# Performance work log

Measured on AMD Instinct MI355X. Metric: run time of the kernel, lower is better.

## Reference

```python
import jax, jax.numpy as jnp
import numpy as np

NODE = 112
L1, L2, L3 = 256, 128, 64
BATCH = 2048


def setup_inputs() -> dict:
    key = jax.random.key(0)
    ks = jax.random.split(key, 19)
    def n(k, shape, s=0.05):
        return jax.random.normal(k, shape, jnp.float32) * s
    return {
        "x": jax.random.uniform(ks[0], (BATCH, NODE, NODE), jnp.float32),
        # GAT1: proj Linear(112->L1); attention Linear(2*L1->1) split into (wa1, wb1, ba1)
        "Wp1": n(ks[1], (L1, NODE)), "bp1": n(ks[2], (L1,)),
        "wa1": n(ks[3], (L1,)), "wb1": n(ks[4], (L1,)), "ba1": n(ks[5], ()),
        # Pool1: proj Linear(L1->1)
        "Wpool1": n(ks[6], (L1,)), "bpool1": n(ks[7], ()),
        # GAT2
        "Wp2": n(ks[8], (L2, L1)), "bp2": n(ks[9], (L2,)),
        "wa2": n(ks[10], (L2,)), "wb2": n(ks[11], (L2,)), "ba2": n(ks[12], ()),
        # Pool2
        "Wpool2": n(ks[13], (L2,)), "bpool2": n(ks[14], ()),
        # FC head
        "Wfc1": n(ks[15], (L3, L2)), "bfc1": n(ks[16], (L3,)),
        "Wfc2": n(ks[17], (1, L3)), "bfc2": n(ks[18], (1,)),
    }


def _gat(a, h, Wp, bp, wa, wb, ba):
    # h: [B,N,Din] -> [B,N,O]
    h = jnp.einsum('bnd,od->bno', h, Wp) + bp
    # attention(concat(h_i, h_j)) == h_i.wa + h_j.wb + ba (linear over concat splits)
    s = jnp.einsum('bno,o->bn', h, wa)  # first-half contribution
    t = jnp.einsum('bno,o->bn', h, wb)  # second-half contribution
    e = jax.nn.relu(s[:, :, None] + t[:, None, :] + ba)  # [B,N,N]
    att = jnp.exp(e) * a
    att = att / jnp.sum(att, axis=-1, keepdims=True)
    return jnp.einsum('bij,bjo->bio', att, h) + h


def _pool(adj, hidden, w, b, k):
    scores = jax.nn.sigmoid(jnp.einsum('bnd,d->bn', hidden, w) + b)  # [B,N]
    vals, idx = jax.lax.top_k(scores, k)  # sorted descending, like torch.topk
    hidden = jnp.take_along_axis(hidden, idx[:, :, None], axis=1) * vals[:, :, None]
    adj = jnp.take_along_axis(adj, idx[:, :, None], axis=1)
    adj = jnp.take_along_axis(adj, idx[:, None, :], axis=2)
    adj = adj / jnp.sum(adj, axis=-1, keepdims=True)
    return adj, hidden


def reference(x, Wp1, bp1, wa1, wb1, ba1, Wpool1, bpool1,
              Wp2, bp2, wa2, wb2, ba2, Wpool2, bpool2,
              Wfc1, bfc1, Wfc2, bfc2):
    b = x.shape[0]
    h = jnp.broadcast_to(jnp.eye(NODE, dtype=x.dtype), (b, NODE, NODE))
    h = jax.nn.relu(_gat(x, h, Wp1, bp1, wa1, wb1, ba1))
    k1 = max(2, int(0.5 * NODE))          # 56
    a, h = _pool(x, h, Wpool1, bpool1, k1)
    h = jax.nn.relu(_gat(a, h, Wp2, bp2, wa2, wb2, ba2))
    k2 = max(2, int(0.5 * k1))            # 28
    a, h = _pool(a, h, Wpool2, bpool2, k2)
    h = jnp.mean(h, axis=1)               # [B,L2]
    h = jax.nn.relu(h @ Wfc1.T + bfc1)
    return h @ Wfc2.T + bfc2              # [B,1]
```

## Files before the change

kernel.cpp:

```cpp
#include <hip/hip_runtime.h>

#define NODE 112
#define KP1 56
#define KP2 28
#define D1 256
#define D2 128
#define NBATCH 2048
#define NCH 4
#define WR 7
#define GR 7
#define CR 28

typedef const float* __restrict__ fp;

__global__ void k0a(fp Wp1, fp bp1, fp wa1, fp wb1,
                    float* __restrict__ s1, float* __restrict__ t1)
{
    int tid = threadIdx.x;
    int i = tid >> 1, half = tid & 1;
    float sa = 0.f, sb = 0.f;
    if (i < NODE) {
        for (int o = half*128; o < half*128 + 128; o++) {
            float h = Wp1[o*NODE + i] + bp1[o];
            sa += h * wa1[o];
            sb += h * wb1[o];
        }
    }
    sa += __shfl_xor(sa, 1, 64);
    sb += __shfl_xor(sb, 1, 64);
    if (i < NODE && half == 0) { s1[i] = sa; t1[i] = sb; }
}

__global__ void k0b(fp Wp1, fp bp1, fp ba1, fp Wp2,
                    const float* __restrict__ s1, const float* __restrict__ t1,
                    float* __restrict__ hp, float* __restrict__ E1, float* __restrict__ W2T)
{
    int g = blockIdx.x*blockDim.x + threadIdx.x;
    int stride = gridDim.x*blockDim.x;
    for (int e = g; e < NODE*D1; e += stride) {
        int j = e >> 8, o = e & 255;
        hp[e] = Wp1[o*NODE + j] + bp1[o];
    }
    float ba = ba1[0];
    for (int e = g; e < NODE*NODE; e += stride) {
        int i = e / NODE, j = e - i*NODE;
        E1[e] = expf(fmaxf(s1[i] + t1[j] + ba, 0.f));
    }
    for (int e = g; e < D1*D2; e += stride) {
        int d = e >> 7, o = e & 127;
        W2T[e] = Wp2[o*D1 + d];
    }
}

__device__ __forceinline__ void topk_wave(volatile float* sc, int n, int k,
                                          int* idxo, float* valo, int tid)
{
    for (int it = 0; it < k; it++) {
        float v = (tid < n) ? sc[tid] : -1e30f;
        int bi = tid;
        int j2 = tid + 64;
        if (j2 < n) { float v2 = sc[j2]; if (v2 > v) { v = v2; bi = j2; } }
        #pragma unroll
        for (int off = 32; off; off >>= 1) {
            float ov = __shfl_xor(v, off, 64);
            int   oi = __shfl_xor(bi, off, 64);
            if (ov > v || (ov == v && oi < bi)) { v = ov; bi = oi; }
        }
        if (tid == 0) { idxo[it] = bi; valo[it] = v; sc[bi] = -1e30f; }
    }
}

__device__ __forceinline__ float sigm(float v) { return 1.f/(1.f + expf(-v)); }

__global__ __launch_bounds__(256, 2) void gnn_fast(
    fp x, fp Wpool1, fp bpool1, fp bp2, fp wa2, fp wb2, fp ba2,
    fp Wpool2, fp bpool2, fp Wfc1, fp bfc1, fp Wfc2, fp bfc2,
    fp hp, fp E1, fp W2T, float* __restrict__ out)
{
    __shared__ __align__(16) float ovl[KP1*D1];
    __shared__ __align__(16) float awc2[KP1*KP1];
    __shared__ float rinv[NODE];
    __shared__ float sc1[NODE];
    __shared__ int   idx1[KP1];
    __shared__ float vals1[KP1];
    __shared__ int   sel[NODE];
    __shared__ float s2v[KP1], t2v[KP1];
    __shared__ float rs2inv[KP1];
    __shared__ float sc2[KP1];
    __shared__ int   idx2[KP2];
    __shared__ float vals2[KP2];
    __shared__ float hmean[D2];

    float* awcF = ovl;
    float* hg   = ovl;

    const int tid = threadIdx.x;
    const int lane = tid & 63, wave = tid >> 6;
    const int b = blockIdx.x;
    const float* xb = x + (size_t)b*NODE*NODE;

    const float4 wp1v = *(const float4*)(Wpool1 + 4*lane);
    const float bpool1v = bpool1[0];

    {
        const int seg = tid & 3;
        #pragma unroll
        for (int pass = 0; pass < 2; pass++) {
            const int i = (tid >> 2) + pass*64;
            float ps = 0.f;
            if (i < NODE) {
                const float4* Er = (const float4*)(E1 + i*NODE + seg*28);
                const float4* xr = (const float4*)(xb + i*NODE + seg*28);
                float4* ar = (float4*)(awcF + i*NODE + seg*28);
                #pragma unroll
                for (int q = 0; q < 7; q++) {
                    float4 e = Er[q], xv = xr[q];
                    float4 v = make_float4(e.x*xv.x, e.y*xv.y, e.z*xv.z, e.w*xv.w);
                    ar[q] = v;
                    ps += (v.x + v.y) + (v.z + v.w);
                }
            }
            ps += __shfl_xor(ps, 1, 64);
            ps += __shfl_xor(ps, 2, 64);
            if (i < NODE && seg == 0) rinv[i] = 1.f/ps;
        }
    }
    __syncthreads();

    const int r0 = wave*WR;
    float h1r[NCH][WR][4];
    #pragma unroll
    for (int c = 0; c < NCH; c++) {
        float acc[WR][4];
        #pragma unroll
        for (int r = 0; r < WR; r++) { acc[r][0]=0.f; acc[r][1]=0.f; acc[r][2]=0.f; acc[r][3]=0.f; }
        #pragma unroll 2
        for (int jq = 0; jq < NODE/4; jq++) {
            const int j = jq*4;
            float4 hv0 = *(const float4*)(hp + (j+0)*D1 + 4*lane);
            float4 hv1 = *(const float4*)(hp + (j+1)*D1 + 4*lane);
            float4 hv2 = *(const float4*)(hp + (j+2)*D1 + 4*lane);
            float4 hv3 = *(const float4*)(hp + (j+3)*D1 + 4*lane);
            #pragma unroll
            for (int r = 0; r < WR; r++) {
                float4 a4 = *(const float4*)&awcF[(c*CR + r0 + r)*NODE + j];
                acc[r][0] += a4.x*hv0.x + a4.y*hv1.x + a4.z*hv2.x + a4.w*hv3.x;
                acc[r][1] += a4.x*hv0.y + a4.y*hv1.y + a4.z*hv2.y + a4.w*hv3.y;
                acc[r][2] += a4.x*hv0.z + a4.y*hv1.z + a4.z*hv2.z + a4.w*hv3.z;
                acc[r][3] += a4.x*hv0.w + a4.y*hv1.w + a4.z*hv2.w + a4.w*hv3.w;
            }
        }
        #pragma unroll
        for (int r = 0; r < WR; r++) {
            const int i = c*CR + r0 + r;
            const float ri = rinv[i];
            float4 hpi = *(const float4*)(hp + i*D1 + 4*lane);
            float v0 = fmaxf(acc[r][0]*ri + hpi.x, 0.f);
            float v1 = fmaxf(acc[r][1]*ri + hpi.y, 0.f);
            float v2 = fmaxf(acc[r][2]*ri + hpi.z, 0.f);
            float v3 = fmaxf(acc[r][3]*ri + hpi.w, 0.f);
            h1r[c][r][0]=v0; h1r[c][r][1]=v1; h1r[c][r][2]=v2; h1r[c][r][3]=v3;
            float p = v0*wp1v.x + v1*wp1v.y + v2*wp1v.z + v3*wp1v.w;
            #pragma unroll
            for (int off = 32; off; off >>= 1) p += __shfl_xor(p, off, 64);
            if (lane == 0) sc1[i] = sigm(p + bpool1v);
        }
    }
    __syncthreads();

    if (tid < 64) topk_wave(sc1, NODE, KP1, idx1, vals1, tid);
    else if (tid >= 128 && tid < 128 + NODE) sel[tid - 128] = -1;
    __syncthreads();
    if (tid < KP1) sel[idx1[tid]] = tid;
    __syncthreads();

    #pragma unroll
    for (int c = 0; c < NCH; c++) {
        #pragma unroll
        for (int r = 0; r < WR; r++) {
            const int i = c*CR + r0 + r;
            const int k = sel[i];
            if (k >= 0) {
                const float vs = vals1[k];
                *(float4*)&hg[k*D1 + 4*lane] =
                    make_float4(h1r[c][r][0]*vs, h1r[c][r][1]*vs,
                                h1r[c][r][2]*vs, h1r[c][r][3]*vs);
            }
        }
    }
    __syncthreads();

    {
        const int g = tid >> 5;
        const int cs = tid & 31;
        float acc2[GR][4];
        #pragma unroll
        for (int r = 0; r < GR; r++) { acc2[r][0]=0.f; acc2[r][1]=0.f; acc2[r][2]=0.f; acc2[r][3]=0.f; }
        #pragma unroll 2
        for (int dq = 0; dq < D1/4; dq++) {
            const int d = dq*4;
            float4 w0 = *(const float4*)(W2T + (d+0)*D2 + 4*cs);
            float4 w1 = *(const float4*)(W2T + (d+1)*D2 + 4*cs);
            float4 w2 = *(const float4*)(W2T + (d+2)*D2 + 4*cs);
            float4 w3 = *(const float4*)(W2T + (d+3)*D2 + 4*cs);
            #pragma unroll
            for (int r = 0; r < GR; r++) {
                float4 a4 = *(const float4*)&hg[(g*GR+r)*D1 + d];
                acc2[r][0] += a4.x*w0.x + a4.y*w1.x + a4.z*w2.x + a4.w*w3.x;
                acc2[r][1] += a4.x*w0.y + a4.y*w1.y + a4.z*w2.y + a4.w*w3.y;
                acc2[r][2] += a4.x*w0.z + a4.y*w1.z + a4.z*w2.z + a4.w*w3.z;
                acc2[r][3] += a4.x*w0.w + a4.y*w1.w + a4.z*w2.w + a4.w*w3.w;
            }
        }
        float4 b2 = *(const float4*)(bp2 + 4*cs);
        __syncthreads();
        #pragma unroll
        for (int r = 0; r < GR; r++) {
            *(float4*)&hg[(g*GR+r)*D1 + 4*cs] =
                make_float4(acc2[r][0]+b2.x, acc2[r][1]+b2.y, acc2[r][2]+b2.z, acc2[r][3]+b2.w);
        }
    }
    __syncthreads();

    if (tid < 4*KP1) {
        int row = tid >> 2, seg = tid & 3;
        float sa = 0.f, sb = 0.f;
        #pragma unroll
        for (int q = 0; q < 8; q++) {
            float4 hv = *(const float4*)&hg[row*D1 + seg*32 + q*4];
            float4 va = *(const float4*)(wa2 + seg*32 + q*4);
            float4 vb = *(const float4*)(wb2 + seg*32 + q*4);
            sa += hv.x*va.x + hv.y*va.y + hv.z*va.z + hv.w*va.w;
            sb += hv.x*vb.x + hv.y*vb.y + hv.z*vb.z + hv.w*vb.w;
        }
        sa += __shfl_xor(sa, 1, 64); sa += __shfl_xor(sa, 2, 64);
        sb += __shfl_xor(sb, 1, 64); sb += __shfl_xor(sb, 2, 64);
        if (seg == 0) { s2v[row] = sa; t2v[row] = sb; }
    }
    __syncthreads();

    if (tid < 4*KP1) {
        int rloc = tid >> 2, seg = tid & 3;
        float ps = 0.f;
        int gi = idx1[rloc];
        float srow = s2v[rloc];
        const float ba2v = ba2[0];
        const float* xrow = xb + gi*NODE;
        float* arow = awc2 + rloc*KP1 + seg*14;
        #pragma unroll
        for (int q = 0; q < 14; q++) {
            int j = seg*14 + q;
            float e = fmaxf(srow + t2v[j] + ba2v, 0.f);
            float v = expf(e) * xrow[idx1[j]];
            arow[q] = v;
            ps += v;
        }
        ps += __shfl_xor(ps, 1, 64); ps += __shfl_xor(ps, 2, 64);
        if (seg == 0) rs2inv[rloc] = 1.f/ps;
    }
    __syncthreads();

    {
        const int g = tid >> 5, cs = tid & 31;
        float acc3[GR][4];
        #pragma unroll
        for (int r = 0; r < GR; r++) { acc3[r][0]=0.f; acc3[r][1]=0.f; acc3[r][2]=0.f; acc3[r][3]=0.f; }
        #pragma unroll 2
        for (int lq = 0; lq < KP1/4; lq++) {
            const int l = lq*4;
            float4 p0 = *(const float4*)&hg[(l+0)*D1 + 4*cs];
            float4 p1 = *(const float4*)&hg[(l+1)*D1 + 4*cs];
            float4 p2 = *(const float4*)&hg[(l+2)*D1 + 4*cs];
            float4 p3 = *(const float4*)&hg[(l+3)*D1 + 4*cs];
            #pragma unroll
            for (int r = 0; r < GR; r++) {
                float4 a4 = *(const float4*)&awc2[(g*GR+r)*KP1 + l];
                acc3[r][0] += a4.x*p0.x + a4.y*p1.x + a4.z*p2.x + a4.w*p3.x;
                acc3[r][1] += a4.x*p0.y + a4.y*p1.y + a4.z*p2.y + a4.w*p3.y;
                acc3[r][2] += a4.x*p0.z + a4.y*p1.z + a4.z*p2.z + a4.w*p3.z;
                acc3[r][3] += a4.x*p0.w + a4.y*p1.w + a4.z*p2.w + a4.w*p3.w;
            }
        }
        const float4 wp2v = *(const float4*)(Wpool2 + 4*cs);
        const float bpool2v = bpool2[0];
        #pragma unroll
        for (int r = 0; r < GR; r++) {
            int row = g*GR + r;
            float ri = rs2inv[row];
            float4 hpj = *(const float4*)&hg[row*D1 + 4*cs];
            float v0 = fmaxf(acc3[r][0]*ri + hpj.x, 0.f);
            float v1 = fmaxf(acc3[r][1]*ri + hpj.y, 0.f);
            float v2 = fmaxf(acc3[r][2]*ri + hpj.z, 0.f);
            float v3 = fmaxf(acc3[r][3]*ri + hpj.w, 0.f);
            *(float4*)&hg[row*D1 + D2 + 4*cs] = make_float4(v0, v1, v2, v3);
            float p = v0*wp2v.x + v1*wp2v.y + v2*wp2v.z + v3*wp2v.w;
            p += __shfl_xor(p, 16, 64); p += __shfl_xor(p, 8, 64);
            p += __shfl_xor(p, 4, 64);  p += __shfl_xor(p, 2, 64);
            p += __shfl_xor(p, 1, 64);
            if (cs == 0) sc2[row] = sigm(p + bpool2v);
        }
    }
    __syncthreads();

    if (tid < 64) topk_wave(sc2, KP1, KP2, idx2, vals2, tid);
    __syncthreads();

    if (tid < D2) {
        float m = 0.f;
        for (int k = 0; k < KP2; k++) m += hg[idx2[k]*D1 + D2 + tid] * vals2[k];
        hmean[tid] = m * (1.f/28.f);
    }
    __syncthreads();

    if (tid < 64) {
        float s = 0.f;
        #pragma unroll
        for (int q = 0; q < 32; q++) {
            float4 w = *(const float4*)(Wfc1 + tid*D2 + q*4);
            s += hmean[q*4+0]*w.x + hmean[q*4+1]*w.y + hmean[q*4+2]*w.z + hmean[q*4+3]*w.w;
        }
        s = fmaxf(s + bfc1[tid], 0.f);
        float v = s * Wfc2[tid];
        #pragma unroll
        for (int off = 32; off; off >>= 1) v += __shfl_xor(v, off, 64);
        if (tid == 0) out[b] = v + bfc2[0];
    }
}

__global__ __launch_bounds__(256) void gnn_fallback(
    fp x, fp Wp1, fp bp1, fp wa1, fp wb1, fp ba1,
    fp Wpool1, fp bpool1, fp Wp2, fp bp2, fp wa2, fp wb2, fp ba2,
    fp Wpool2, fp bpool2, fp Wfc1, fp bfc1, fp Wfc2, fp bfc2,
    float* __restrict__ out)
{
    __shared__ __align__(16) float hg[KP1*D1];
    __shared__ __align__(16) float awc[CR*NODE];
    __shared__ float s1v[NODE], t1v[NODE];
    __shared__ float sc1[NODE];
    __shared__ float rsc[KP1];
    __shared__ float redc[4*CR];
    __shared__ int   idx1[KP1];
    __shared__ float vals1[KP1];
    __shared__ float s2v[KP1], t2v[KP1];
    __shared__ float sc2[KP1];
    __shared__ int   idx2[KP2];
    __shared__ float vals2[KP2];
    __shared__ float hmean[D2];

    const int tid = threadIdx.x;
    const int lane = tid & 63, wave = tid >> 6;
    const int b = blockIdx.x;
    const float* xb = x + (size_t)b*NODE*NODE;

    const float wpool1v = Wpool1[tid];
    const float bpool1v = bpool1[0];
    const float ba1v    = ba1[0];
    const float* wrow = Wp1 + tid*NODE;
    const float bp1v = bp1[tid];

    if (tid < NODE) {
        float sa = 0.f, sb = 0.f;
        for (int o = 0; o < D1; o++) {
            float h = Wp1[o*NODE + tid] + bp1[o];
            sa += h * wa1[o];
            sb += h * wb1[o];
        }
        s1v[tid] = sa; t1v[tid] = sb;
    }
    __syncthreads();

    for (int c = 0; c < NODE/CR; c++) {
        const int i0 = c*CR;
        for (int e = tid; e < CR*NODE; e += 256) {
            int r = e / NODE, j = e - r*NODE;
            int i = i0 + r;
            float ee = fmaxf(s1v[i] + t1v[j] + ba1v, 0.f);
            awc[e] = expf(ee) * xb[i*NODE + j];
        }
        __syncthreads();
        if (tid < CR) {
            float s = 0.f;
            for (int j = 0; j < NODE; j++) s += awc[tid*NODE + j];
            rsc[tid] = s;
        }
        __syncthreads();
        float acc[CR];
        #pragma unroll
        for (int r = 0; r < CR; r++) acc[r] = 0.f;
        for (int jg = 0; jg < NODE/4; jg++) {
            float4 w = *(const float4*)(wrow + jg*4);
            float h0 = w.x + bp1v, h1 = w.y + bp1v, h2 = w.z + bp1v, h3 = w.w + bp1v;
            #pragma unroll
            for (int r = 0; r < CR; r++) {
                float4 a4 = *(const float4*)&awc[r*NODE + jg*4];
                acc[r] += a4.x*h0 + a4.y*h1 + a4.z*h2 + a4.w*h3;
            }
        }
        float part[CR];
        #pragma unroll
        for (int r = 0; r < CR; r++) {
            float hpi = wrow[i0 + r] + bp1v;
            float h1v = fmaxf(acc[r]/rsc[r] + hpi, 0.f);
            part[r] = h1v * wpool1v;
        }
        #pragma unroll
        for (int r = 0; r < CR; r++) {
            float v = part[r];
            #pragma unroll
            for (int off = 32; off; off >>= 1) v += __shfl_xor(v, off, 64);
            if (lane == 0) redc[wave*CR + r] = v;
        }
        __syncthreads();
        if (tid < CR) {
            float s = redc[tid] + redc[CR+tid] + redc[2*CR+tid] + redc[3*CR+tid];
            sc1[i0 + tid] = sigm(s + bpool1v);
        }
        __syncthreads();
    }

    if (tid < 64) topk_wave(sc1, NODE, KP1, idx1, vals1, tid);
    __syncthreads();

    for (int c = 0; c < KP1/CR; c++) {
        const int k0 = c*CR;
        for (int e = tid; e < CR*NODE; e += 256) {
            int r = e / NODE, j = e - r*NODE;
            int i = idx1[k0 + r];
            float ee = fmaxf(s1v[i] + t1v[j] + ba1v, 0.f);
            awc[e] = expf(ee) * xb[i*NODE + j];
        }
        __syncthreads();
        if (tid < CR) {
            float s = 0.f;
            for (int j = 0; j < NODE; j++) s += awc[tid*NODE + j];
            rsc[tid] = s;
        }
        __syncthreads();
        float acc[CR];
        #pragma unroll
        for (int r = 0; r < CR; r++) acc[r] = 0.f;
        for (int jg = 0; jg < NODE/4; jg++) {
            float4 w = *(const float4*)(wrow + jg*4);
            float h0 = w.x + bp1v, h1 = w.y + bp1v, h2 = w.z + bp1v, h3 = w.w + bp1v;
            #pragma unroll
            for (int r = 0; r < CR; r++) {
                float4 a4 = *(const float4*)&awc[r*NODE + jg*4];
                acc[r] += a4.x*h0 + a4.y*h1 + a4.z*h2 + a4.w*h3;
            }
        }
        #pragma unroll
        for (int r = 0; r < CR; r++) {
            int k = k0 + r;
            float hpi = wrow[idx1[k]] + bp1v;
            float h1v = fmaxf(acc[r]/rsc[r] + hpi, 0.f);
            hg[k*D1 + tid] = h1v * vals1[k];
        }
        __syncthreads();
    }

    {
        const int half = tid >> 7, o = tid & 127;
        const float* w2row = Wp2 + o*D1;
        float acc2[CR];
        #pragma unroll
        for (int r = 0; r < CR; r++) acc2[r] = 0.f;
        for (int d4 = 0; d4 < D1; d4 += 4) {
            float4 w = *(const float4*)(w2row + d4);
            #pragma unroll
            for (int r = 0; r < CR; r++) {
                float4 h4 = *(const float4*)&hg[(half*CR + r)*D1 + d4];
                acc2[r] += h4.x*w.x + h4.y*w.y + h4.z*w.z + h4.w*w.w;
            }
        }
        __syncthreads();
        float bp2v = bp2[o];
        #pragma unroll
        for (int r = 0; r < CR; r++)
            hg[(half*CR + r)*D1 + o] = acc2[r] + bp2v;
    }
    __syncthreads();

    if (tid < KP1) {
        float sa = 0.f, sb = 0.f;
        for (int o2 = 0; o2 < D2; o2++) {
            float hv = hg[tid*D1 + o2];
            sa += hv * wa2[o2];
            sb += hv * wb2[o2];
        }
        s2v[tid] = sa; t2v[tid] = sb;
    }
    __syncthreads();

    {
        const float ba2v = ba2[0];
        for (int e = tid; e < KP1*KP1; e += 256) {
            int i = e / KP1, j = e - i*KP1;
            float ee = fmaxf(s2v[i] + t2v[j] + ba2v, 0.f);
            awc[e] = expf(ee) * xb[idx1[i]*NODE + idx1[j]];
        }
    }
    __syncthreads();
    if (tid < KP1) {
        float s = 0.f;
        for (int j = 0; j < KP1; j++) s += awc[tid*KP1 + j];
        rsc[tid] = s;
    }
    __syncthreads();

    {
        const int half = tid >> 7, o = tid & 127;
        float acc3[CR];
        #pragma unroll
        for (int r = 0; r < CR; r++) acc3[r] = 0.f;
        for (int l4 = 0; l4 < KP1; l4 += 4) {
            float p0 = hg[(l4+0)*D1 + o];
            float p1 = hg[(l4+1)*D1 + o];
            float p2 = hg[(l4+2)*D1 + o];
            float p3 = hg[(l4+3)*D1 + o];
            #pragma unroll
            for (int r = 0; r < CR; r++) {
                float4 a4 = *(const float4*)&awc[(half*CR + r)*KP1 + l4];
                acc3[r] += a4.x*p0 + a4.y*p1 + a4.z*p2 + a4.w*p3;
            }
        }
        const float wpool2v = Wpool2[o];
        float part2[CR];
        #pragma unroll
        for (int r = 0; r < CR; r++) {
            int n = half*CR + r;
            float h2v = fmaxf(acc3[r]/rsc[n] + hg[n*D1 + o], 0.f);
            hg[n*D1 + D2 + o] = h2v;
            part2[r] = h2v * wpool2v;
        }
        #pragma unroll
        for (int r = 0; r < CR; r++) {
            float v = part2[r];
            #pragma unroll
            for (int off = 32; off; off >>= 1) v += __shfl_xor(v, off, 64);
            if (lane == 0) redc[wave*CR + r] = v;
        }
    }
    __syncthreads();
    {
        const float bpool2v = bpool2[0];
        if (tid < KP1) {
            int hh = tid / CR, rr = tid - hh*CR;
            float s = redc[(2*hh)*CR + rr] + redc[(2*hh+1)*CR + rr];
            sc2[tid] = sigm(s + bpool2v);
        }
    }
    __syncthreads();

    if (tid < 64) topk_wave(sc2, KP1, KP2, idx2, vals2, tid);
    __syncthreads();

    if (tid < D2) {
        float m = 0.f;
        for (int k = 0; k < KP2; k++) m += hg[idx2[k]*D1 + D2 + tid] * vals2[k];
        hmean[tid] = m * (1.f/28.f);
    }
    __syncthreads();

    if (tid < 64) {
        float s = 0.f;
        for (int d = 0; d < D2; d++) s += hmean[d] * Wfc1[tid*D2 + d];
        s = fmaxf(s + bfc1[tid], 0.f);
        float v = s * Wfc2[tid];
        #pragma unroll
        for (int off = 32; off; off >>= 1) v += __shfl_xor(v, off, 64);
        if (tid == 0) out[b] = v + bfc2[0];
    }
}

extern "C" void kernel_launch(void* const* d_in, const int* in_sizes, int n_in,
                              void* d_out, int out_size, void* d_ws, size_t ws_size,
                              hipStream_t stream) {
    (void)in_sizes; (void)n_in; (void)out_size;
    fp x      = (fp)d_in[0];
    fp Wp1    = (fp)d_in[1];
    fp bp1    = (fp)d_in[2];
    fp wa1    = (fp)d_in[3];
    fp wb1    = (fp)d_in[4];
    fp ba1    = (fp)d_in[5];
    fp Wpool1 = (fp)d_in[6];
    fp bpool1 = (fp)d_in[7];
    fp Wp2    = (fp)d_in[8];
    fp bp2    = (fp)d_in[9];
    fp wa2    = (fp)d_in[10];
    fp wb2    = (fp)d_in[11];
    fp ba2    = (fp)d_in[12];
    fp Wpool2 = (fp)d_in[13];
    fp bpool2 = (fp)d_in[14];
    fp Wfc1   = (fp)d_in[15];
    fp bfc1   = (fp)d_in[16];
    fp Wfc2   = (fp)d_in[17];
    fp bfc2   = (fp)d_in[18];

    const size_t WS_NEED = (size_t)(NODE*D1 + NODE*NODE + D1*D2 + 2*NODE) * sizeof(float);

    if (ws_size >= WS_NEED) {
        float* hp  = (float*)d_ws;
        float* E1  = hp  + NODE*D1;
        float* W2T = E1  + NODE*NODE;
        float* s1  = W2T + D1*D2;
        float* t1  = s1  + NODE;
        hipLaunchKernelGGL(k0a, dim3(1), dim3(256), 0, stream,
                           Wp1, bp1, wa1, wb1, s1, t1);
        hipLaunchKernelGGL(k0b, dim3(64), dim3(256), 0, stream,
                           Wp1, bp1, ba1, Wp2, s1, t1, hp, E1, W2T);
        hipLaunchKernelGGL(gnn_fast, dim3(NBATCH), dim3(256), 0, stream,
                           x, Wpool1, bpool1, bp2, wa2, wb2, ba2,
                           Wpool2, bpool2, Wfc1, bfc1, Wfc2, bfc2,
                           hp, E1, W2T, (float*)d_out);
    } else {
        hipLaunchKernelGGL(gnn_fallback, dim3(NBATCH), dim3(256), 0, stream,
                           x, Wp1, bp1, wa1, wb1, ba1, Wpool1, bpool1,
                           Wp2, bp2, wa2, wb2, ba2, Wpool2, bpool2,
                           Wfc1, bfc1, Wfc2, bfc2, (float*)d_out);
    }
}
```

Measured before the change: 754.1 us.

## Shrink shared memory by splitting GAT2 projection into halves to fit three blocks

The shared buffer is shrunk from KP1*D1 plus KP1*KP1 floats to NODE*NODE floats. To make this fit, the pooled layer-1 features are staged in two 128-column halves, and the GAT2 projection accumulates over each half in turn. Layer-2 outputs now stay in registers and are scattered into a compact selected buffer after top-k, and launch bounds are raised to 3 blocks per CU. The aim is higher occupancy, at the cost of extra barriers, a second staging pass and more register pressure from holding h2v, which could cause spills.

```diff
diff --git a/kernel.cpp b/kernel.cpp
--- a/kernel.cpp
+++ b/kernel.cpp
@@ -72,13 +72,12 @@
 
 __device__ __forceinline__ float sigm(float v) { return 1.f/(1.f + expf(-v)); }
 
-__global__ __launch_bounds__(256, 2) void gnn_fast(
+__global__ __launch_bounds__(256, 3) void gnn_fast(
     fp x, fp Wpool1, fp bpool1, fp bp2, fp wa2, fp wb2, fp ba2,
     fp Wpool2, fp bpool2, fp Wfc1, fp bfc1, fp Wfc2, fp bfc2,
     fp hp, fp E1, fp W2T, float* __restrict__ out)
 {
-    __shared__ __align__(16) float ovl[KP1*D1];
-    __shared__ __align__(16) float awc2[KP1*KP1];
+    __shared__ __align__(16) float ovl[NODE*NODE];
     __shared__ float rinv[NODE];
     __shared__ float sc1[NODE];
     __shared__ int   idx1[KP1];
@@ -91,8 +90,11 @@
     __shared__ float vals2[KP2];
     __shared__ float hmean[D2];
 
-    float* awcF = ovl;
-    float* hg   = ovl;
+    float* awcF   = ovl;
+    float* hb     = ovl;
+    float* h2proj = ovl;
+    float* att2   = ovl + KP1*D2;
+    float* h2sel  = ovl + KP1*D2;
 
     const int tid = threadIdx.x;
     const int lane = tid & 63, wave = tid >> 6;
@@ -174,49 +176,81 @@
     if (tid < KP1) sel[idx1[tid]] = tid;
     __syncthreads();
 
+    float acc2[GR][4];
+    #pragma unroll
+    for (int r = 0; r < GR; r++) { acc2[r][0]=0.f; acc2[r][1]=0.f; acc2[r][2]=0.f; acc2[r][3]=0.f; }
+    const int g = tid >> 5;
+    const int cs = tid & 31;
+
     #pragma unroll
     for (int c = 0; c < NCH; c++) {
         #pragma unroll
         for (int r = 0; r < WR; r++) {
             const int i = c*CR + r0 + r;
             const int k = sel[i];
-            if (k >= 0) {
+            if (k >= 0 && lane < 32) {
                 const float vs = vals1[k];
-                *(float4*)&hg[k*D1 + 4*lane] =
+                *(float4*)&hb[k*D2 + 4*lane] =
                     make_float4(h1r[c][r][0]*vs, h1r[c][r][1]*vs,
                                 h1r[c][r][2]*vs, h1r[c][r][3]*vs);
             }
         }
     }
     __syncthreads();
-
+    #pragma unroll 2
+    for (int dq = 0; dq < 32; dq++) {
+        const int d = dq*4;
+        float4 w0 = *(const float4*)(W2T + (d+0)*D2 + 4*cs);
+        float4 w1 = *(const float4*)(W2T + (d+1)*D2 + 4*cs);
+        float4 w2 = *(const float4*)(W2T + (d+2)*D2 + 4*cs);
+        float4 w3 = *(const float4*)(W2T + (d+3)*D2 + 4*cs);
+        #pragma unroll
+        for (int r = 0; r < GR; r++) {
+            float4 a4 = *(const float4*)&hb[(g*GR+r)*D2 + d];
+            acc2[r][0] += a4.x*w0.x + a4.y*w1.x + a4.z*w2.x + a4.w*w3.x;
+            acc2[r][1] += a4.x*w0.y + a4.y*w1.y + a4.z*w2.y + a4.w*w3.y;
+            acc2[r][2] += a4.x*w0.z + a4.y*w1.z + a4.z*w2.z + a4.w*w3.z;
+            acc2[r][3] += a4.x*w0.w + a4.y*w1.w + a4.z*w2.w + a4.w*w3.w;
+        }
+    }
+    __syncthreads();
+    #pragma unroll
+    for (int c = 0; c < NCH; c++) {
+        #pragma unroll
+        for (int r = 0; r < WR; r++) {
+            const int i = c*CR + r0 + r;
+            const int k = sel[i];
+            if (k >= 0 && lane >= 32) {
+                const float vs = vals1[k];
+                *(float4*)&hb[k*D2 + 4*lane - 128] =
+                    make_float4(h1r[c][r][0]*vs, h1r[c][r][1]*vs,
+                                h1r[c][r][2]*vs, h1r[c][r][3]*vs);
+            }
+        }
+    }
+    __syncthreads();
+    #pragma unroll 2
+    for (int dq = 0; dq < 32; dq++) {
+        const int d = dq*4;
+        float4 w0 = *(const float4*)(W2T + (128+d+0)*D2 + 4*cs);
+        float4 w1 = *(const float4*)(W2T + (128+d+1)*D2 + 4*cs);
+        float4 w2 = *(const float4*)(W2T + (128+d+2)*D2 + 4*cs);
+        float4 w3 = *(const float4*)(W2T + (128+d+3)*D2 + 4*cs);
+        #pragma unroll
+        for (int r = 0; r < GR; r++) {
+            float4 a4 = *(const float4*)&hb[(g*GR+r)*D2 + d];
+            acc2[r][0] += a4.x*w0.x + a4.y*w1.x + a4.z*w2.x + a4.w*w3.x;
+            acc2[r][1] += a4.x*w0.y + a4.y*w1.y + a4.z*w2.y + a4.w*w3.y;
+            acc2[r][2] += a4.x*w0.z + a4.y*w1.z + a4.z*w2.z + a4.w*w3.z;
+            acc2[r][3] += a4.x*w0.w + a4.y*w1.w + a4.z*w2.w + a4.w*w3.w;
+        }
+    }
+    __syncthreads();
     {
-        const int g = tid >> 5;
-        const int cs = tid & 31;
-        float acc2[GR][4];
-        #pragma unroll
-        for (int r = 0; r < GR; r++) { acc2[r][0]=0.f; acc2[r][1]=0.f; acc2[r][2]=0.f; acc2[r][3]=0.f; }
-        #pragma unroll 2
-        for (int dq = 0; dq < D1/4; dq++) {
-            const int d = dq*4;
-            float4 w0 = *(const float4*)(W2T + (d+0)*D2 + 4*cs);
-            float4 w1 = *(const float4*)(W2T + (d+1)*D2 + 4*cs);
-            float4 w2 = *(const float4*)(W2T + (d+2)*D2 + 4*cs);
-            float4 w3 = *(const float4*)(W2T + (d+3)*D2 + 4*cs);
-            #pragma unroll
-            for (int r = 0; r < GR; r++) {
-                float4 a4 = *(const float4*)&hg[(g*GR+r)*D1 + d];
-                acc2[r][0] += a4.x*w0.x + a4.y*w1.x + a4.z*w2.x + a4.w*w3.x;
-                acc2[r][1] += a4.x*w0.y + a4.y*w1.y + a4.z*w2.y + a4.w*w3.y;
-                acc2[r][2] += a4.x*w0.z + a4.y*w1.z + a4.z*w2.z + a4.w*w3.z;
-                acc2[r][3] += a4.x*w0.w + a4.y*w1.w + a4.z*w2.w + a4.w*w3.w;
-            }
-        }
         float4 b2 = *(const float4*)(bp2 + 4*cs);
-        __syncthreads();
         #pragma unroll
         for (int r = 0; r < GR; r++) {
-            *(float4*)&hg[(g*GR+r)*D1 + 4*cs] =
+            *(float4*)&h2proj[(g*GR+r)*D2 + 4*cs] =
                 make_float4(acc2[r][0]+b2.x, acc2[r][1]+b2.y, acc2[r][2]+b2.z, acc2[r][3]+b2.w);
         }
     }
@@ -227,7 +261,7 @@
         float sa = 0.f, sb = 0.f;
         #pragma unroll
         for (int q = 0; q < 8; q++) {
-            float4 hv = *(const float4*)&hg[row*D1 + seg*32 + q*4];
+            float4 hv = *(const float4*)&h2proj[row*D2 + seg*32 + q*4];
             float4 va = *(const float4*)(wa2 + seg*32 + q*4);
             float4 vb = *(const float4*)(wb2 + seg*32 + q*4);
             sa += hv.x*va.x + hv.y*va.y + hv.z*va.z + hv.w*va.w;
@@ -246,7 +280,7 @@
         float srow = s2v[rloc];
         const float ba2v = ba2[0];
         const float* xrow = xb + gi*NODE;
-        float* arow = awc2 + rloc*KP1 + seg*14;
+        float* arow = att2 + rloc*KP1 + seg*14;
         #pragma unroll
         for (int q = 0; q < 14; q++) {
             int j = seg*14 + q;
@@ -260,21 +294,21 @@
     }
     __syncthreads();
 
+    float h2v[GR][4];
     {
-        const int g = tid >> 5, cs = tid & 31;
         float acc3[GR][4];
         #pragma unroll
         for (int r = 0; r < GR; r++) { acc3[r][0]=0.f; acc3[r][1]=0.f; acc3[r][2]=0.f; acc3[r][3]=0.f; }
         #pragma unroll 2
         for (int lq = 0; lq < KP1/4; lq++) {
             const int l = lq*4;
-            float4 p0 = *(const float4*)&hg[(l+0)*D1 + 4*cs];
-            float4 p1 = *(const float4*)&hg[(l+1)*D1 + 4*cs];
-            float4 p2 = *(const float4*)&hg[(l+2)*D1 + 4*cs];
-            float4 p3 = *(const float4*)&hg[(l+3)*D1 + 4*cs];
+            float4 p0 = *(const float4*)&h2proj[(l+0)*D2 + 4*cs];
+            float4 p1 = *(const float4*)&h2proj[(l+1)*D2 + 4*cs];
+            float4 p2 = *(const float4*)&h2proj[(l+2)*D2 + 4*cs];
+            float4 p3 = *(const float4*)&h2proj[(l+3)*D2 + 4*cs];
             #pragma unroll
             for (int r = 0; r < GR; r++) {
-                float4 a4 = *(const float4*)&awc2[(g*GR+r)*KP1 + l];
+                float4 a4 = *(const float4*)&att2[(g*GR+r)*KP1 + l];
                 acc3[r][0] += a4.x*p0.x + a4.y*p1.x + a4.z*p2.x + a4.w*p3.x;
                 acc3[r][1] += a4.x*p0.y + a4.y*p1.y + a4.z*p2.y + a4.w*p3.y;
                 acc3[r][2] += a4.x*p0.z + a4.y*p1.z + a4.z*p2.z + a4.w*p3.z;
@@ -287,12 +321,12 @@
         for (int r = 0; r < GR; r++) {
             int row = g*GR + r;
             float ri = rs2inv[row];
-            float4 hpj = *(const float4*)&hg[row*D1 + 4*cs];
+            float4 hpj = *(const float4*)&h2proj[row*D2 + 4*cs];
             float v0 = fmaxf(acc3[r][0]*ri + hpj.x, 0.f);
             float v1 = fmaxf(acc3[r][1]*ri + hpj.y, 0.f);
             float v2 = fmaxf(acc3[r][2]*ri + hpj.z, 0.f);
             float v3 = fmaxf(acc3[r][3]*ri + hpj.w, 0.f);
-            *(float4*)&hg[row*D1 + D2 + 4*cs] = make_float4(v0, v1, v2, v3);
+            h2v[r][0]=v0; h2v[r][1]=v1; h2v[r][2]=v2; h2v[r][3]=v3;
             float p = v0*wp2v.x + v1*wp2v.y + v2*wp2v.z + v3*wp2v.w;
             p += __shfl_xor(p, 16, 64); p += __shfl_xor(p, 8, 64);
             p += __shfl_xor(p, 4, 64);  p += __shfl_xor(p, 2, 64);
@@ -303,11 +337,27 @@
     __syncthreads();
 
     if (tid < 64) topk_wave(sc2, KP1, KP2, idx2, vals2, tid);
+    else if (tid >= 128 && tid < 128 + KP1) sel[tid - 128] = -1;
+    __syncthreads();
+    if (tid < KP2) sel[idx2[tid]] = tid;
+    __syncthreads();
+
+    #pragma unroll
+    for (int r = 0; r < GR; r++) {
+        const int row = g*GR + r;
+        const int kk = sel[row];
+        if (kk >= 0) {
+            const float vs = vals2[kk];
+            *(float4*)&h2sel[kk*D2 + 4*cs] =
+                make_float4(h2v[r][0]*vs, h2v[r][1]*vs, h2v[r][2]*vs, h2v[r][3]*vs);
+        }
+    }
     __syncthreads();
 
     if (tid < D2) {
         float m = 0.f;
-        for (int k = 0; k < KP2; k++) m += hg[idx2[k]*D1 + D2 + tid] * vals2[k];
+        #pragma unroll
+        for (int k = 0; k < KP2; k++) m += h2sel[k*D2 + tid];
         hmean[tid] = m * (1.f/28.f);
     }
     __syncthreads();
```

Measured after the change: 786.5 us. 1.04x slower.
